# Performance work log

Hardware: AMD Instinct MI355X
Metric: run time of the kernel (lower is better)

Reference implementation:

```python
import jax, jax.numpy as jnp
import numpy as np


def setup_inputs() -> dict:
    key = jax.random.key(0)
    k1, k2, k3 = jax.random.split(key, 3)
    B, T, F, U = 32, 4096, 512, 512
    x = jax.random.normal(k1, (B, T, F), dtype=jnp.float32)
    W = jax.random.normal(k2, (F, U), dtype=jnp.float32)
    b = jnp.zeros((U,), dtype=jnp.float32)
    V = jax.random.uniform(k3, (U, 1), dtype=jnp.float32)
    return {"x": x, "W": W, "b": b, "V": V}


def reference(x, W, b, V):
    # u = tanh(x @ W + b): [B, T, U]
    u = jnp.tanh(jnp.einsum('btf,fu->btu', x, W) + b)
    # scores = u @ V: [B, T, 1]; softmax over time (dim=1)
    a = jax.nn.softmax(jnp.einsum('btu,uo->bto', u, V), axis=1)
    # weighted sum pooling over time -> [B, F]
    return jnp.sum(x * a, axis=1)
```

## Files before the change

kernel.cpp:

```cpp
#include <hip/hip_runtime.h>


#define XT 4096
#define XF 512
#define XU 512

typedef __attribute__((ext_vector_type(8))) short short8;
typedef __attribute__((ext_vector_type(16))) float f32x16;

__device__ inline void cvt_hilo(float x, unsigned short &h, unsigned short &l) {
  unsigned u = __builtin_bit_cast(unsigned, x);
  h = (unsigned short)(u >> 16);
  float hf = __builtin_bit_cast(float, u & 0xFFFF0000u);
  float lo = x - hf;
  l = (unsigned short)(__builtin_bit_cast(unsigned, lo) >> 16);
}

__device__ inline float tanh_fast(float z) {
  float e = __expf(2.0f * z);
  return 1.0f - 2.0f * __builtin_amdgcn_rcpf(e + 1.0f);
}

__global__ void wconv_kernel(const float *__restrict__ W,
                             unsigned short *__restrict__ whi,
                             unsigned short *__restrict__ wlo) {
  int t2 = blockIdx.x * 256 + threadIdx.x;
  int l = t2 & 31;
  int g = (t2 >> 5) & 1;
  int t = (t2 >> 6) & 15;
  int s = t2 >> 10;
  short8 hv, lv;
#pragma unroll
  for (int j = 0; j < 8; ++j) {
    unsigned short h, lo;
    cvt_hilo(W[(size_t)(s * 16 + g * 8 + j) * XU + t * 32 + l], h, lo);
    hv[j] = (short)h;
    lv[j] = (short)lo;
  }
  size_t off = (size_t)s * 8192 + t * 512 + g * 256 + l * 8;
  *(short8 *)(whi + off) = hv;
  *(short8 *)(wlo + off) = lv;
}

#define MFMA(a, b, c) __builtin_amdgcn_mfma_f32_32x32x16_bf16(a, b, c, 0, 0, 0)

__global__ __launch_bounds__(512, 2)
void gemm_scores_kernel(const float *__restrict__ x,
                        const unsigned short *__restrict__ whi,
                        const unsigned short *__restrict__ wlo,
                        const float *__restrict__ bias,
                        const float *__restrict__ V,
                        float *__restrict__ partial,
                        float *__restrict__ pstats) {
  __shared__ unsigned short Bsh[2][4][8192];
  __shared__ float scb[256];
  __shared__ float sarr[128];
  __shared__ float warr[128];
  __shared__ float red[1536];

  const int tid = threadIdx.x;
  const int lane = tid & 63;
  const int wave = tid >> 6;
  const int rs = wave & 3;
  const int c = wave >> 2;
  const int l31 = lane & 31;
  const int half = lane >> 5;
  const size_t rowbase = (size_t)blockIdx.x * 128;

  f32x16 acc[8];
#pragma unroll
  for (int cf = 0; cf < 8; ++cf)
#pragma unroll
    for (int r = 0; r < 16; ++r) acc[cf][r] = 0.f;

  const float *xr = x + (rowbase + rs * 32 + l31) * XF + half * 8;
  const int toff = tid * 8;
  const int fbase = (c * 8) * 512 + lane * 8;

  short8 st0, st1, st2, st3, st4, st5, st6, st7;
  float4 xa0, xa1, xa2, xa3;

#define LOADSTG(J)                                                   \
  {                                                                  \
    const unsigned short *ph = whi + (size_t)(2 * (J)) * 8192;       \
    const unsigned short *pl = wlo + (size_t)(2 * (J)) * 8192;       \
    st0 = *(const short8 *)(ph + toff);                              \
    st1 = *(const short8 *)(ph + 4096 + toff);                       \
    st2 = *(const short8 *)(pl + toff);                              \
    st3 = *(const short8 *)(pl + 4096 + toff);                       \
    st4 = *(const short8 *)(ph + 8192 + toff);                       \
    st5 = *(const short8 *)(ph + 12288 + toff);                      \
    st6 = *(const short8 *)(pl + 8192 + toff);                       \
    st7 = *(const short8 *)(pl + 12288 + toff);                      \
  }
#define WRITESTG(BUF)                                                \
  {                                                                  \
    unsigned short *d = &Bsh[BUF][0][0] + toff;                      \
    *(short8 *)(d) = st0;                                            \
    *(short8 *)(d + 4096) = st1;                                     \
    *(short8 *)(d + 8192) = st2;                                     \
    *(short8 *)(d + 12288) = st3;                                    \
    *(short8 *)(d + 16384) = st4;                                    \
    *(short8 *)(d + 20480) = st5;                                    \
    *(short8 *)(d + 24576) = st6;                                    \
    *(short8 *)(d + 28672) = st7;                                    \
  }
#define LOADA(J)                                                     \
  {                                                                  \
    xa0 = *(const float4 *)(xr + (J) * 32);                          \
    xa1 = *(const float4 *)(xr + (J) * 32 + 4);                      \
    xa2 = *(const float4 *)(xr + (J) * 32 + 16);                     \
    xa3 = *(const float4 *)(xr + (J) * 32 + 20);                     \
  }

  LOADSTG(0);
  LOADA(0);
  WRITESTG(0);
  __syncthreads();

#pragma unroll 1
  for (int j = 0; j < 16; ++j) {
    const int cur = j & 1;

    short8 ah0, al0, ah1, al1;
    {
      float v0[8] = {xa0.x, xa0.y, xa0.z, xa0.w, xa1.x, xa1.y, xa1.z, xa1.w};
      float v1[8] = {xa2.x, xa2.y, xa2.z, xa2.w, xa3.x, xa3.y, xa3.z, xa3.w};
#pragma unroll
      for (int jj = 0; jj < 8; ++jj) {
        unsigned short h, lo;
        cvt_hilo(v0[jj], h, lo);
        ah0[jj] = (short)h; al0[jj] = (short)lo;
        cvt_hilo(v1[jj], h, lo);
        ah1[jj] = (short)h; al1[jj] = (short)lo;
      }
    }

    if (j < 15) {
      LOADSTG(j + 1);
      LOADA(j + 1);
    }

#pragma unroll
    for (int h = 0; h < 2; ++h) {
      const unsigned short *bp = &Bsh[cur][h * 2][0] + fbase;
      const unsigned short *lp = bp + 8192;
      short8 ahf = h ? ah1 : ah0;
      short8 alf = h ? al1 : al0;
#pragma unroll
      for (int cf = 0; cf < 8; ++cf) {
        short8 bh = *(const short8 *)(bp + cf * 512);
        short8 bl = *(const short8 *)(lp + cf * 512);
        acc[cf] = MFMA(ahf, bh, acc[cf]);
        acc[cf] = MFMA(alf, bh, acc[cf]);
        acc[cf] = MFMA(ahf, bl, acc[cf]);
      }
    }

    if (j < 15) WRITESTG(cur ^ 1);
    __syncthreads();
  }

  float sc[16];
#pragma unroll
  for (int r = 0; r < 16; ++r) sc[r] = 0.f;
#pragma unroll
  for (int cf = 0; cf < 8; ++cf) {
    int n = c * 256 + cf * 32 + l31;
    float vv = V[n];
    float bb = bias[n];
#pragma unroll
    for (int r = 0; r < 16; ++r)
      sc[r] += tanh_fast(acc[cf][r] + bb) * vv;
  }
#pragma unroll
  for (int m = 1; m <= 16; m <<= 1) {
#pragma unroll
    for (int r = 0; r < 16; ++r) sc[r] += __shfl_xor(sc[r], m, 64);
  }
  if (l31 == 0) {
#pragma unroll
    for (int r = 0; r < 16; ++r) {
      int row = rs * 32 + (r & 3) + 8 * (r >> 2) + 4 * half;
      scb[c * 128 + row] = sc[r];
    }
  }
  __syncthreads();

  if (tid < 128) sarr[tid] = scb[tid] + scb[128 + tid];
  __syncthreads();
  float mloc = -1e30f;
#pragma unroll 8
  for (int i = 0; i < 128; ++i) mloc = fmaxf(mloc, sarr[i]);
  if (tid < 128) warr[tid] = __expf(sarr[tid] - mloc);
  __syncthreads();

  float lsum = 0.f;
  if (tid < 64) {
    lsum = warr[tid] + warr[tid + 64];
#pragma unroll
    for (int m = 1; m < 64; m <<= 1) lsum += __shfl_xor(lsum, m, 64);
  }

  const int rg = tid >> 7;
  const int c4 = tid & 127;
  const float *xp = x + rowbase * XF;
  float4 pa = {0.f, 0.f, 0.f, 0.f};
#pragma unroll 8
  for (int i = 0; i < 32; ++i) {
    int r = rg * 32 + i;
    float4 v = *(const float4 *)(xp + (size_t)r * XF + c4 * 4);
    float wv = warr[r];
    pa.x += wv * v.x;
    pa.y += wv * v.y;
    pa.z += wv * v.z;
    pa.w += wv * v.w;
  }
  if (rg > 0) {
    float *rp = red + (rg - 1) * 512 + c4 * 4;
    rp[0] = pa.x; rp[1] = pa.y; rp[2] = pa.z; rp[3] = pa.w;
  }
  __syncthreads();
  if (rg == 0) {
    const float *r0 = red + c4 * 4;
    float4 o;
    o.x = pa.x + r0[0] + r0[512] + r0[1024];
    o.y = pa.y + r0[1] + r0[513] + r0[1025];
    o.z = pa.z + r0[2] + r0[514] + r0[1026];
    o.w = pa.w + r0[3] + r0[515] + r0[1027];
    *(float4 *)(partial + (size_t)blockIdx.x * 512 + c4 * 4) = o;
  }
  if (tid == 0) {
    pstats[blockIdx.x * 2] = mloc;
    pstats[blockIdx.x * 2 + 1] = lsum;
  }
}

__global__ __launch_bounds__(512)
void combine_kernel(const float *__restrict__ partial,
                    const float *__restrict__ pstats,
                    float *__restrict__ out) {
  int b = blockIdx.x;
  int f = threadIdx.x;
  __shared__ float ml[32], ll[32];
  if (f < 32) {
    ml[f] = pstats[(b * 32 + f) * 2];
    ll[f] = pstats[(b * 32 + f) * 2 + 1];
  }
  __syncthreads();
  float M = -1e30f;
#pragma unroll
  for (int c = 0; c < 32; ++c) M = fmaxf(M, ml[c]);
  float L = 0.f;
#pragma unroll
  for (int c = 0; c < 32; ++c) L += __expf(ml[c] - M) * ll[c];
  float acc = 0.f;
#pragma unroll
  for (int c = 0; c < 32; ++c)
    acc += __expf(ml[c] - M) * partial[(size_t)(b * 32 + c) * 512 + f];
  out[b * XF + f] = acc / L;
}

extern "C" void kernel_launch(void *const *d_in, const int *in_sizes, int n_in,
                              void *d_out, int out_size, void *d_ws,
                              size_t ws_size, hipStream_t stream) {
  const float *x = (const float *)d_in[0];
  const float *W = (const float *)d_in[1];
  const float *bias = (const float *)d_in[2];
  const float *V = (const float *)d_in[3];
  float *out = (float *)d_out;

  unsigned short *whi = (unsigned short *)d_ws;
  unsigned short *wlo = whi + 262144;
  float *partial = (float *)((char *)d_ws + 1048576);
  float *pstats = (float *)((char *)d_ws + 1048576 + 2097152);

  wconv_kernel<<<128, 256, 0, stream>>>(W, whi, wlo);
  gemm_scores_kernel<<<1024, 512, 0, stream>>>(x, whi, wlo, bias, V, partial,
                                               pstats);
  combine_kernel<<<32, 512, 0, stream>>>(partial, pstats, out);
}
```

Baseline: 527.7 us.

## Stage W tiles via direct global-to-LDS loads and software-pipeline LDS fragment reads

Replaces the register-staged global loads and LDS writes of the bf16 hi/lo W tiles with global_load_lds direct-to-LDS transfers into a double buffer. LDS fragment reads are split into sub-blocks that are prefetched one cluster ahead of the MFMA groups, including the first sub-block of the next iteration after the barrier. MFMA clusters are wrapped in s_setprio to favour matrix issue. The goal is to cut VGPR staging, VALU store traffic and LDS read latency exposed to the MFMA pipe. The cost is more fragment registers and a dependence on the barrier correctly covering the asynchronous LDS writes.

Result: slower. 545.9 us (+3.5%).

```diff
diff --git a/kernel.cpp b/kernel.cpp
--- a/kernel.cpp
+++ b/kernel.cpp
@@ -19,6 +19,13 @@
 __device__ inline float tanh_fast(float z) {
   float e = __expf(2.0f * z);
   return 1.0f - 2.0f * __builtin_amdgcn_rcpf(e + 1.0f);
+}
+
+__device__ inline void load_lds_16B(const unsigned short *gsrc,
+                                    unsigned short *ldst) {
+  __builtin_amdgcn_global_load_lds(
+      (const __attribute__((address_space(1))) unsigned int *)gsrc,
+      (__attribute__((address_space(3))) unsigned int *)ldst, 16, 0, 0);
 }
 
 __global__ void wconv_kernel(const float *__restrict__ W,
@@ -44,6 +51,39 @@
 
 #define MFMA(a, b, c) __builtin_amdgcn_mfma_f32_32x32x16_bf16(a, b, c, 0, 0, 0)
 
+#define READSUB(BASE, H, CFG, SET)                                  \
+  {                                                                 \
+    const unsigned short *bp_ = (BASE) + (H)*16384 + (CFG)*2048 + fbase; \
+    Fh##SET[0] = *(const short8 *)(bp_);                            \
+    Fh##SET[1] = *(const short8 *)(bp_ + 512);                      \
+    Fh##SET[2] = *(const short8 *)(bp_ + 1024);                     \
+    Fh##SET[3] = *(const short8 *)(bp_ + 1536);                     \
+    Fl##SET[0] = *(const short8 *)(bp_ + 8192);                     \
+    Fl##SET[1] = *(const short8 *)(bp_ + 8704);                     \
+    Fl##SET[2] = *(const short8 *)(bp_ + 9216);                     \
+    Fl##SET[3] = *(const short8 *)(bp_ + 9728);                     \
+  }
+
+#define CLUSTER(H, CFG, SET)                                        \
+  {                                                                 \
+    short8 aH_ = (H) ? ah1 : ah0;                                   \
+    short8 aL_ = (H) ? al1 : al0;                                   \
+    __builtin_amdgcn_s_setprio(1);                                  \
+    acc[(CFG)*4 + 0] = MFMA(aH_, Fh##SET[0], acc[(CFG)*4 + 0]);     \
+    acc[(CFG)*4 + 0] = MFMA(aL_, Fh##SET[0], acc[(CFG)*4 + 0]);     \
+    acc[(CFG)*4 + 0] = MFMA(aH_, Fl##SET[0], acc[(CFG)*4 + 0]);     \
+    acc[(CFG)*4 + 1] = MFMA(aH_, Fh##SET[1], acc[(CFG)*4 + 1]);     \
+    acc[(CFG)*4 + 1] = MFMA(aL_, Fh##SET[1], acc[(CFG)*4 + 1]);     \
+    acc[(CFG)*4 + 1] = MFMA(aH_, Fl##SET[1], acc[(CFG)*4 + 1]);     \
+    acc[(CFG)*4 + 2] = MFMA(aH_, Fh##SET[2], acc[(CFG)*4 + 2]);     \
+    acc[(CFG)*4 + 2] = MFMA(aL_, Fh##SET[2], acc[(CFG)*4 + 2]);     \
+    acc[(CFG)*4 + 2] = MFMA(aH_, Fl##SET[2], acc[(CFG)*4 + 2]);     \
+    acc[(CFG)*4 + 3] = MFMA(aH_, Fh##SET[3], acc[(CFG)*4 + 3]);     \
+    acc[(CFG)*4 + 3] = MFMA(aL_, Fh##SET[3], acc[(CFG)*4 + 3]);     \
+    acc[(CFG)*4 + 3] = MFMA(aH_, Fl##SET[3], acc[(CFG)*4 + 3]);     \
+    __builtin_amdgcn_s_setprio(0);                                  \
+  }
+
 __global__ __launch_bounds__(512, 2)
 void gemm_scores_kernel(const float *__restrict__ x,
                         const unsigned short *__restrict__ whi,
@@ -52,7 +92,7 @@
                         const float *__restrict__ V,
                         float *__restrict__ partial,
                         float *__restrict__ pstats) {
-  __shared__ unsigned short Bsh[2][4][8192];
+  __shared__ unsigned short Bsh[2][32768];
   __shared__ float scb[256];
   __shared__ float sarr[128];
   __shared__ float warr[128];
@@ -74,55 +114,32 @@
     for (int r = 0; r < 16; ++r) acc[cf][r] = 0.f;
 
   const float *xr = x + (rowbase + rs * 32 + l31) * XF + half * 8;
-  const int toff = tid * 8;
-  const int fbase = (c * 8) * 512 + lane * 8;
-
-  short8 st0, st1, st2, st3, st4, st5, st6, st7;
+  const int fbase = c * 4096 + lane * 8;
+
+  const int w2 = wave >> 1;
+  const unsigned short *gsrc0 = ((w2 & 1) ? wlo : whi) +
+                                (size_t)(w2 >> 1) * 8192 + (wave & 1) * 4096 +
+                                lane * 8;
+  unsigned short *ldsW = &Bsh[0][0] + w2 * 8192 + (wave & 1) * 4096;
+  unsigned short *Bsh0 = &Bsh[0][0];
+
+  short8 Fh0[4], Fl0[4], Fh1[4], Fl1[4];
   float4 xa0, xa1, xa2, xa3;
-
-#define LOADSTG(J)                                                   \
-  {                                                                  \
-    const unsigned short *ph = whi + (size_t)(2 * (J)) * 8192;       \
-    const unsigned short *pl = wlo + (size_t)(2 * (J)) * 8192;       \
-    st0 = *(const short8 *)(ph + toff);                              \
-    st1 = *(const short8 *)(ph + 4096 + toff);                       \
-    st2 = *(const short8 *)(pl + toff);                              \
-    st3 = *(const short8 *)(pl + 4096 + toff);                       \
-    st4 = *(const short8 *)(ph + 8192 + toff);                       \
-    st5 = *(const short8 *)(ph + 12288 + toff);                      \
-    st6 = *(const short8 *)(pl + 8192 + toff);                       \
-    st7 = *(const short8 *)(pl + 12288 + toff);                      \
-  }
-#define WRITESTG(BUF)                                                \
-  {                                                                  \
-    unsigned short *d = &Bsh[BUF][0][0] + toff;                      \
-    *(short8 *)(d) = st0;                                            \
-    *(short8 *)(d + 4096) = st1;                                     \
-    *(short8 *)(d + 8192) = st2;                                     \
-    *(short8 *)(d + 12288) = st3;                                    \
-    *(short8 *)(d + 16384) = st4;                                    \
-    *(short8 *)(d + 20480) = st5;                                    \
-    *(short8 *)(d + 24576) = st6;                                    \
-    *(short8 *)(d + 28672) = st7;                                    \
-  }
-#define LOADA(J)                                                     \
-  {                                                                  \
-    xa0 = *(const float4 *)(xr + (J) * 32);                          \
-    xa1 = *(const float4 *)(xr + (J) * 32 + 4);                      \
-    xa2 = *(const float4 *)(xr + (J) * 32 + 16);                     \
-    xa3 = *(const float4 *)(xr + (J) * 32 + 20);                     \
-  }
-
-  LOADSTG(0);
-  LOADA(0);
-  WRITESTG(0);
-  __syncthreads();
+  short8 ah0, al0, ah1, al1;
+
+#pragma unroll
+  for (int i = 0; i < 8; ++i) load_lds_16B(gsrc0 + i * 512, ldsW + i * 512);
+  xa0 = *(const float4 *)(xr);
+  xa1 = *(const float4 *)(xr + 4);
+  xa2 = *(const float4 *)(xr + 16);
+  xa3 = *(const float4 *)(xr + 20);
+  __syncthreads();
+  READSUB(Bsh0, 0, 0, 0);
 
 #pragma unroll 1
   for (int j = 0; j < 16; ++j) {
-    const int cur = j & 1;
-
-    short8 ah0, al0, ah1, al1;
+    const unsigned short *bsC = Bsh0 + (j & 1) * 32768;
+
     {
       float v0[8] = {xa0.x, xa0.y, xa0.z, xa0.w, xa1.x, xa1.y, xa1.z, xa1.w};
       float v1[8] = {xa2.x, xa2.y, xa2.z, xa2.w, xa3.x, xa3.y, xa3.z, xa3.w};
@@ -137,28 +154,29 @@
     }
 
     if (j < 15) {
-      LOADSTG(j + 1);
-      LOADA(j + 1);
+      const unsigned short *gs = gsrc0 + (size_t)(j + 1) * 16384;
+      unsigned short *ls = ldsW + ((j + 1) & 1) * 32768;
+#pragma unroll
+      for (int i = 0; i < 8; ++i) load_lds_16B(gs + i * 512, ls + i * 512);
+      xa0 = *(const float4 *)(xr + (j + 1) * 32);
+      xa1 = *(const float4 *)(xr + (j + 1) * 32 + 4);
+      xa2 = *(const float4 *)(xr + (j + 1) * 32 + 16);
+      xa3 = *(const float4 *)(xr + (j + 1) * 32 + 20);
     }
 
-#pragma unroll
-    for (int h = 0; h < 2; ++h) {
-      const unsigned short *bp = &Bsh[cur][h * 2][0] + fbase;
-      const unsigned short *lp = bp + 8192;
-      short8 ahf = h ? ah1 : ah0;
-      short8 alf = h ? al1 : al0;
-#pragma unroll
-      for (int cf = 0; cf < 8; ++cf) {
-        short8 bh = *(const short8 *)(bp + cf * 512);
-        short8 bl = *(const short8 *)(lp + cf * 512);
-        acc[cf] = MFMA(ahf, bh, acc[cf]);
-        acc[cf] = MFMA(alf, bh, acc[cf]);
-        acc[cf] = MFMA(ahf, bl, acc[cf]);
-      }
+    READSUB(bsC, 0, 1, 1);
+    CLUSTER(0, 0, 0);
+    READSUB(bsC, 1, 0, 0);
+    CLUSTER(0, 1, 1);
+    READSUB(bsC, 1, 1, 1);
+    CLUSTER(1, 0, 0);
+    CLUSTER(1, 1, 1);
+
+    __syncthreads();
+    if (j < 15) {
+      const unsigned short *bsN = Bsh0 + ((j + 1) & 1) * 32768;
+      READSUB(bsN, 0, 0, 0);
     }
-
-    if (j < 15) WRITESTG(cur ^ 1);
-    __syncthreads();
   }
 
   float sc[16];
```
